# Kernel tuning notes

Hardware: AMD Instinct MI355X
Metric: run time of the kernel (lower is better)

Reference implementation:

```python
import jax, jax.numpy as jnp
import numpy as np

B, S, HID = 1, 2048, 2048
NH, NKV, D = 32, 8, 64
GROUPS = NH // NKV
THETA = 10000.0


def _rope_tables(seq_len, dim):
    inv_freq = 1.0 / (THETA ** (jnp.arange(0, dim, 2, dtype=jnp.float32) / dim))
    t = jnp.arange(seq_len, dtype=jnp.float32)
    freqs = jnp.outer(t, inv_freq)            # [S, D/2]
    emb = jnp.concatenate([freqs, freqs], axis=-1)  # [S, D]
    return jnp.cos(emb), jnp.sin(emb)


def _rotate_half(x):
    x1, x2 = jnp.split(x, 2, axis=-1)
    return jnp.concatenate([-x2, x1], axis=-1)


def setup_inputs() -> dict:
    key = jax.random.key(0)
    ks = jax.random.split(key, 8)
    hidden_states = jax.random.normal(ks[0], (B, S, HID), dtype=jnp.float32)
    # additive causal mask, 0 on/below diagonal, -1e9 above
    causal = jnp.tril(jnp.ones((S, S), dtype=bool))
    attention_mask = jnp.where(causal, 0.0, -1e9).astype(jnp.float32)[None, None]
    sc = 0.02
    Wq = sc * jax.random.normal(ks[1], (NH * D, HID), dtype=jnp.float32)
    bq = jnp.zeros((NH * D,), dtype=jnp.float32)
    Wk = sc * jax.random.normal(ks[2], (NKV * D, HID), dtype=jnp.float32)
    bk = jnp.zeros((NKV * D,), dtype=jnp.float32)
    Wv = sc * jax.random.normal(ks[3], (NKV * D, HID), dtype=jnp.float32)
    bv = jnp.zeros((NKV * D,), dtype=jnp.float32)
    Wo = sc * jax.random.normal(ks[4], (HID, NH * D), dtype=jnp.float32)
    return {"hidden_states": hidden_states, "attention_mask": attention_mask,
            "Wq": Wq, "bq": bq, "Wk": Wk, "bk": bk, "Wv": Wv, "bv": bv, "Wo": Wo}


def reference(hidden_states, attention_mask, Wq, bq, Wk, bk, Wv, bv, Wo):
    b, s, _ = hidden_states.shape
    q = (hidden_states @ Wq.T + bq).reshape(b, s, NH, D).transpose(0, 2, 1, 3)   # [B,NH,S,D]
    k = (hidden_states @ Wk.T + bk).reshape(b, s, NKV, D).transpose(0, 2, 1, 3)  # [B,NKV,S,D]
    v = (hidden_states @ Wv.T + bv).reshape(b, s, NKV, D).transpose(0, 2, 1, 3)
    cos, sin = _rope_tables(s, D)
    cos = cos[None, None]; sin = sin[None, None]
    q = q * cos + _rotate_half(q) * sin
    k = k * cos + _rotate_half(k) * sin
    # GQA: repeat KV heads to match query heads
    k = jnp.repeat(k, GROUPS, axis=1)  # [B,NH,S,D]
    v = jnp.repeat(v, GROUPS, axis=1)
    scores = jnp.einsum('bhqd,bhkd->bhqk', q, k) / jnp.sqrt(jnp.float32(D))
    scores = jnp.clip(scores, -50.0, 50.0)
    scores = scores + attention_mask
    probs = jax.nn.softmax(scores.astype(jnp.float32), axis=-1).astype(q.dtype)
    attn = jnp.einsum('bhqk,bhkd->bhqd', probs, v)
    attn = attn.transpose(0, 2, 1, 3).reshape(b, s, NH * D)
    return attn @ Wo.T
```

## Files before the change

kernel.cpp:

```cpp
#include <hip/hip_runtime.h>
#include <hip/hip_bf16.h>
#include <stdint.h>

typedef unsigned short u16;
typedef unsigned int u32;

#define S_LEN 2048
#define HID 2048
#define NH 32
#define NKV 8
#define HD 64
#define PIT 2080

using f32x4 = __attribute__((ext_vector_type(4))) float;
using bfrag = __attribute__((ext_vector_type(8))) short;

__device__ __forceinline__ float b2f(u16 u) {
  union { u32 i; float f; } c; c.i = ((u32)u) << 16; return c.f;
}
__device__ __forceinline__ u16 f2b(float f) {
  union { float f; u32 i; } c; c.f = f;
  u32 r = c.i + 0x7fffu + ((c.i >> 16) & 1u);
  return (u16)(r >> 16);
}
__device__ __forceinline__ uint4 cvt8(const float* __restrict__ p) {
  float4 a = *(const float4*)p;
  float4 b = *(const float4*)(p + 4);
  uint4 r;
  r.x = (u32)f2b(a.x) | ((u32)f2b(a.y) << 16);
  r.y = (u32)f2b(a.z) | ((u32)f2b(a.w) << 16);
  r.z = (u32)f2b(b.x) | ((u32)f2b(b.y) << 16);
  r.w = (u32)f2b(b.z) | ((u32)f2b(b.w) << 16);
  return r;
}

__device__ __forceinline__ void gl2lds16(const u16* g, u16* l) {
  __builtin_amdgcn_global_load_lds(
      (const __attribute__((address_space(1))) void*)g,
      (__attribute__((address_space(3))) void*)l,
      16, 0, 0);
}

#define WAITBAR(N) asm volatile("s_waitcnt vmcnt(" #N ")\ns_barrier" ::: "memory")

__global__ void conv_all(const float* __restrict__ hid, const float* __restrict__ Wq,
                         const float* __restrict__ Wk, const float* __restrict__ Wv,
                         u16* __restrict__ hidb, u16* __restrict__ Wqkvb) {
  int row = blockIdx.x;
  int col = threadIdx.x * 8;
  const float* src; u16* dst;
  if (row < 2048)      { src = hid + (size_t)row * 2048;          dst = hidb  + (size_t)row * PIT; }
  else if (row < 4096) { src = Wq + (size_t)(row - 2048) * 2048;  dst = Wqkvb + (size_t)(row - 2048) * PIT; }
  else if (row < 4608) { src = Wk + (size_t)(row - 4096) * 2048;  dst = Wqkvb + (size_t)(row - 4096 + 2048) * PIT; }
  else                 { src = Wv + (size_t)(row - 4608) * 2048;  dst = Wqkvb + (size_t)(row - 4608 + 2560) * PIT; }
  *(uint4*)(dst + col) = cvt8(src + col);
}

__global__ void conv_f2b_p(const float* __restrict__ in, u16* __restrict__ out, int n8) {
  int i = blockIdx.x * 256 + threadIdx.x;
  if (i >= n8) return;
  int row = i >> 8;
  int col = (i & 255) * 8;
  *(uint4*)(out + (size_t)row * PIT + col) = cvt8(in + (size_t)row * 2048 + col);
}

__global__ __launch_bounds__(256, 3) void gemm_qkv(
    const u16* __restrict__ A, const u16* __restrict__ B,
    const float* __restrict__ bq, const float* __restrict__ bk, const float* __restrict__ bv,
    u16* __restrict__ Qb, u16* __restrict__ Kb, u16* __restrict__ Vt)
{
  __shared__ __align__(16) u16 As[3 * 2048];
  __shared__ __align__(16) u16 Bs[3 * 4096];
  __shared__ __align__(16) u16 strip_s[4][16 * 72];

  const int tid  = threadIdx.x;
  const int m0   = blockIdx.y * 64;
  const int n0   = blockIdx.x * 128;
  const int lane = tid & 63;
  const int w    = tid >> 6;
  const int wm   = w >> 1, wn = w & 1;
  const int quad = lane >> 4, l16 = lane & 15;

  const int srow = tid >> 2;
  const int scol = (tid & 3) * 8;
  const u16* ga = A + (size_t)(m0 + srow) * PIT + scol;
  const u16* gb = B + (size_t)(n0 + srow) * PIT + scol;

#define STAGE_G(bi, k0)                                                         \
  do {                                                                          \
    gl2lds16(ga + (k0), As + (bi) * 2048 + tid * 8);                            \
    gl2lds16(gb + (k0), Bs + (bi) * 4096 + tid * 8);                            \
    gl2lds16(gb + (size_t)64 * PIT + (k0), Bs + (bi) * 4096 + 2048 + tid * 8);  \
  } while (0)

  f32x4 zero = {0.f, 0.f, 0.f, 0.f};
  f32x4 acc[2][4];
#pragma unroll
  for (int mi = 0; mi < 2; ++mi)
#pragma unroll
    for (int ni = 0; ni < 4; ++ni) acc[mi][ni] = zero;

  STAGE_G(0, 0);
  STAGE_G(1, 32);

  int cur = 0;
  for (int k = 0; k < 64; ++k) {
    if (k < 63) WAITBAR(3);
    else        WAITBAR(0);
    if (k + 2 < 64) {
      int nb = cur + 2; if (nb >= 3) nb -= 3;
      STAGE_G(nb, (k + 2) * 32);
    }
    const u16* as = As + cur * 2048;
    const u16* bs = Bs + cur * 4096;

    bfrag af[2], bf[4];
#pragma unroll
    for (int i = 0; i < 2; ++i)
      af[i] = *(const bfrag*)&as[(wm * 32 + i * 16 + l16) * 32 + quad * 8];
#pragma unroll
    for (int i = 0; i < 4; ++i)
      bf[i] = *(const bfrag*)&bs[(wn * 64 + i * 16 + l16) * 32 + quad * 8];
#pragma unroll
    for (int mi = 0; mi < 2; ++mi)
#pragma unroll
      for (int ni = 0; ni < 4; ++ni)
        acc[mi][ni] = __builtin_amdgcn_mfma_f32_16x16x32_bf16(af[mi], bf[ni], acc[mi][ni], 0, 0, 0);

    cur += 1; if (cur == 3) cur = 0;
  }
#undef STAGE_G

  u16* strip = strip_s[w];
  const int rr = lane >> 2;
  const int co = (lane & 3) * 8;

  if (n0 < 2048) {
#pragma unroll
    for (int mi = 0; mi < 2; ++mi) {
#pragma unroll
      for (int n01 = 0; n01 < 2; ++n01)
#pragma unroll
        for (int i = 0; i < 4; ++i) {
          int d  = n01 * 16 + l16;
          int c1 = n0 + wn * 64 + d;
          float x1 = acc[mi][n01][i]     + bq[c1];
          float x2 = acc[mi][n01 + 2][i] + bq[c1 + 32];
          float inv = exp2f(-(float)d * 0.41524101186092034f);
          float ang = (float)(m0 + wm * 32 + mi * 16 + quad * 4 + i) * inv;
          float cs = cosf(ang), sn = sinf(ang);
          strip[(quad * 4 + i) * 72 + d]      = f2b(x1 * cs - x2 * sn);
          strip[(quad * 4 + i) * 72 + d + 32] = f2b(x2 * cs + x1 * sn);
        }
      uint4 v0 = *(const uint4*)&strip[rr * 72 + co];
      uint4 v1 = *(const uint4*)&strip[rr * 72 + 32 + co];
      size_t gb2 = (size_t)(m0 + wm * 32 + mi * 16 + rr) * 2048 + n0 + wn * 64;
      *(uint4*)(Qb + gb2 + co)      = v0;
      *(uint4*)(Qb + gb2 + 32 + co) = v1;
    }
  } else if (n0 < 2560) {
    int cb = (n0 - 2048) + wn * 64;
#pragma unroll
    for (int mi = 0; mi < 2; ++mi) {
#pragma unroll
      for (int n01 = 0; n01 < 2; ++n01)
#pragma unroll
        for (int i = 0; i < 4; ++i) {
          int d  = n01 * 16 + l16;
          int cg = cb + d;
          float x1 = acc[mi][n01][i]     + bk[cg];
          float x2 = acc[mi][n01 + 2][i] + bk[cg + 32];
          float inv = exp2f(-(float)d * 0.41524101186092034f);
          float ang = (float)(m0 + wm * 32 + mi * 16 + quad * 4 + i) * inv;
          float cs = cosf(ang), sn = sinf(ang);
          strip[(quad * 4 + i) * 72 + d]      = f2b(x1 * cs - x2 * sn);
          strip[(quad * 4 + i) * 72 + d + 32] = f2b(x2 * cs + x1 * sn);
        }
      uint4 v0 = *(const uint4*)&strip[rr * 72 + co];
      uint4 v1 = *(const uint4*)&strip[rr * 72 + 32 + co];
      size_t gb2 = (size_t)(m0 + wm * 32 + mi * 16 + rr) * 512 + cb;
      *(uint4*)(Kb + gb2 + co)      = v0;
      *(uint4*)(Kb + gb2 + 32 + co) = v1;
    }
  } else {
    int cgb = (n0 - 2560) + wn * 64;
#pragma unroll
    for (int ni = 0; ni < 4; ++ni) {
      float bvv = bv[cgb + ni * 16 + l16];
#pragma unroll
      for (int mi = 0; mi < 2; ++mi)
#pragma unroll
        for (int i = 0; i < 4; ++i)
          strip[l16 * 72 + mi * 16 + quad * 4 + i] = f2b(acc[mi][ni][i] + bvv);
      uint4 v0 = *(const uint4*)&strip[rr * 72 + co];
      size_t gb2 = (size_t)(cgb + ni * 16 + rr) * PIT + m0 + wm * 32;
      *(uint4*)(Vt + gb2 + co) = v0;
    }
  }
}

__global__ __launch_bounds__(256, 3) void gemm_o(
    const u16* __restrict__ A, const u16* __restrict__ B, float* __restrict__ C)
{
  __shared__ __align__(16) u16 As[2 * 4096];
  __shared__ __align__(16) u16 Bs[2 * 8192];

  const int tid  = threadIdx.x;
  const int m0   = blockIdx.y * 64;
  const int n0   = blockIdx.x * 128;
  const int lane = tid & 63;
  const int w    = tid >> 6;
  const int wm   = w >> 1, wn = w & 1;
  const int quad = lane >> 4, l16 = lane & 15;

  const int sr = tid >> 3;
  const int sg = (tid & 7) ^ (sr & 7);
  const u16* gA = A + (size_t)(m0 + sr) * PIT + sg * 8;
  const u16* gB = B + (size_t)(n0 + sr) * PIT + sg * 8;

#define STAGE_O(bi, k0)                                                          \
  do {                                                                           \
    gl2lds16(gA + (k0),                    As + (bi) * 4096 + tid * 8);          \
    gl2lds16(gA + (size_t)32 * PIT + (k0), As + (bi) * 4096 + 2048 + tid * 8);   \
    gl2lds16(gB + (k0),                    Bs + (bi) * 8192 + tid * 8);          \
    gl2lds16(gB + (size_t)32 * PIT + (k0), Bs + (bi) * 8192 + 2048 + tid * 8);   \
    gl2lds16(gB + (size_t)64 * PIT + (k0), Bs + (bi) * 8192 + 4096 + tid * 8);   \
    gl2lds16(gB + (size_t)96 * PIT + (k0), Bs + (bi) * 8192 + 6144 + tid * 8);   \
  } while (0)

  f32x4 zero = {0.f, 0.f, 0.f, 0.f};
  f32x4 acc[2][4];
#pragma unroll
  for (int mi = 0; mi < 2; ++mi)
#pragma unroll
    for (int ni = 0; ni < 4; ++ni) acc[mi][ni] = zero;

  STAGE_O(0, 0);

  int cur = 0;
  for (int k = 0; k < 32; ++k) {
    WAITBAR(0);
    if (k + 1 < 32) STAGE_O(cur ^ 1, (k + 1) * 64);
    const u16* as = As + cur * 4096;
    const u16* bs = Bs + cur * 8192;

#pragma unroll
    for (int kk = 0; kk < 2; ++kk) {
      const int sA = ((kk * 4 + quad) ^ (l16 & 7)) * 8;
      bfrag af[2], bf[4];
#pragma unroll
      for (int i = 0; i < 2; ++i)
        af[i] = *(const bfrag*)&as[(wm * 32 + i * 16 + l16) * 64 + sA];
#pragma unroll
      for (int i = 0; i < 4; ++i)
        bf[i] = *(const bfrag*)&bs[(wn * 64 + i * 16 + l16) * 64 + sA];
#pragma unroll
      for (int mi = 0; mi < 2; ++mi)
#pragma unroll
        for (int ni = 0; ni < 4; ++ni)
          acc[mi][ni] = __builtin_amdgcn_mfma_f32_16x16x32_bf16(af[mi], bf[ni], acc[mi][ni], 0, 0, 0);
    }
    cur ^= 1;
  }
#undef STAGE_O

#pragma unroll
  for (int ni = 0; ni < 4; ++ni) {
    int col = n0 + wn * 64 + ni * 16 + l16;
#pragma unroll
    for (int mi = 0; mi < 2; ++mi)
#pragma unroll
      for (int i = 0; i < 4; ++i) {
        int row = m0 + wm * 32 + mi * 16 + quad * 4 + i;
        C[(size_t)row * 2048 + col] = acc[mi][ni][i];
      }
  }
}

#define SM_SC 0.18033688011112042f
#define SM_UB 72.134752044448169f

__global__ __launch_bounds__(256, 2) void attn_flash6(
    const u16* __restrict__ Qb, const u16* __restrict__ Kb,
    const u16* __restrict__ Vt, u16* __restrict__ Ab)
{
  __shared__ __align__(16) u16 Ks[3][64 * 64];
  __shared__ __align__(16) u16 Vs[3][64 * 64];
  __shared__ __align__(16) u16 Ps[4][16][72];

  const int h    = blockIdx.x;
  const int p    = blockIdx.y;
  const int kvh  = h >> 2;
  const int tid  = threadIdx.x;
  const int lane = tid & 63;
  const int w    = tid >> 6;
  const int quad = lane >> 4, l16 = lane & 15;

  const int qtA = 31 - p, qtB = p;
  const int nA  = qtA + 1;

  const int c0  = w * 128 + lane;
  const int r0  = c0 >> 3,        s0 = c0 & 7;
  const int r1  = (c0 + 64) >> 3, s1 = (c0 + 64) & 7;
  const int sg0 = s0 ^ (r0 & 7);
  const int sg1 = s1 ^ (r1 & 7);
  const u16* Ksrc0 = Kb + (size_t)r0 * 512 + kvh * 64 + sg0 * 8;
  const u16* Ksrc1 = Kb + (size_t)r1 * 512 + kvh * 64 + sg1 * 8;
  const u16* Vsrc0 = Vt + (size_t)(kvh * 64 + r0) * PIT + sg0 * 8;
  const u16* Vsrc1 = Vt + (size_t)(kvh * 64 + r1) * PIT + sg1 * 8;

#define STAGEKV(buf, kb)                                                        \
  do {                                                                          \
    gl2lds16(Ksrc0 + (size_t)(kb) * 32768, &Ks[buf][0] + c0 * 8);               \
    gl2lds16(Ksrc1 + (size_t)(kb) * 32768, &Ks[buf][0] + (c0 + 64) * 8);        \
    gl2lds16(Vsrc0 + (kb) * 64,            &Vs[buf][0] + c0 * 8);               \
    gl2lds16(Vsrc1 + (kb) * 64,            &Vs[buf][0] + (c0 + 64) * 8);        \
  } while (0)

  STAGEKV(0, 0);
  STAGEKV(1, 1);

  bfrag qfA0, qfA1, qfB0, qfB1;
  {
    const u16* qa = Qb + (size_t)(qtA * 64 + w * 16 + l16) * 2048 + h * 64 + quad * 8;
    const u16* qb = Qb + (size_t)(qtB * 64 + w * 16 + l16) * 2048 + h * 64 + quad * 8;
    qfA0 = *(const bfrag*)qa;  qfA1 = *(const bfrag*)(qa + 32);
    qfB0 = *(const bfrag*)qb;  qfB1 = *(const bfrag*)(qb + 32);
  }
  bfrag q0 = qfA0, q1 = qfA1;

  f32x4 zero = {0.f, 0.f, 0.f, 0.f};
  f32x4 o_acc[4];
  float lpart[4];
#pragma unroll
  for (int nb = 0; nb < 4; ++nb) { o_acc[nb] = zero; lpart[nb] = 0.f; }

  const int swz = (l16 & 7) * 8;
  int qt = qtA;
  int cur = 0;

  for (int t = 0; t < 33; ++t) {
    if (t < 32) WAITBAR(4);
    else        WAITBAR(0);
    if (t + 2 < 33) {
      int kb2 = (t + 2 < nA) ? (t + 2) : (t + 2 - nA);
      int b3 = cur + 2; if (b3 >= 3) b3 -= 3;
      STAGEKV(b3, kb2);
    }
    if (t == nA) { q0 = qfB0; q1 = qfB1; qt = qtB; }

    const u16* ks = &Ks[cur][0];
    const u16* vs = &Vs[cur][0];

    bfrag kf0[4], kf1[4];
#pragma unroll
    for (int nb = 0; nb < 4; ++nb) {
      int row = (nb * 16 + l16) * 64;
      kf0[nb] = *(const bfrag*)&ks[row + ((quad * 8) ^ swz)];
      kf1[nb] = *(const bfrag*)&ks[row + ((32 + quad * 8) ^ swz)];
    }

    const bool diag = (t == nA - 1) || (t == 32);

    f32x4 s_acc[4];
#pragma unroll
    for (int nb = 0; nb < 4; ++nb) {
      s_acc[nb] = __builtin_amdgcn_mfma_f32_16x16x32_bf16(q0, kf0[nb], zero, 0, 0, 0);
      s_acc[nb] = __builtin_amdgcn_mfma_f32_16x16x32_bf16(q1, kf1[nb], s_acc[nb], 0, 0, 0);
    }
    if (diag) {
#pragma unroll
      for (int nb = 0; nb < 4; ++nb)
#pragma unroll
        for (int i = 0; i < 4; ++i) {
          float u = s_acc[nb][i] * SM_SC;
          u = fminf(SM_UB, fmaxf(-SM_UB, u));
          bool msk = (nb * 16 + l16 > w * 16 + quad * 4 + i);
          float pr = msk ? 0.0f : __builtin_amdgcn_exp2f(u);
          lpart[i] += pr;
          Ps[w][quad * 4 + i][nb * 16 + l16] = f2b(pr);
        }
    } else {
#pragma unroll
      for (int nb = 0; nb < 4; ++nb)
#pragma unroll
        for (int i = 0; i < 4; ++i) {
          float u = s_acc[nb][i] * SM_SC;
          u = fminf(SM_UB, fmaxf(-SM_UB, u));
          float pr = __builtin_amdgcn_exp2f(u);
          lpart[i] += pr;
          Ps[w][quad * 4 + i][nb * 16 + l16] = f2b(pr);
        }
    }

    bfrag vf0[4], vf1[4];
#pragma unroll
    for (int nb = 0; nb < 4; ++nb) {
      int row = (nb * 16 + l16) * 64;
      vf0[nb] = *(const bfrag*)&vs[row + ((quad * 8) ^ swz)];
      vf1[nb] = *(const bfrag*)&vs[row + ((32 + quad * 8) ^ swz)];
    }
    {
      bfrag pf0 = *(const bfrag*)&Ps[w][l16][quad * 8];
      bfrag pf1 = *(const bfrag*)&Ps[w][l16][32 + quad * 8];
#pragma unroll
      for (int nb = 0; nb < 4; ++nb) {
        o_acc[nb] = __builtin_amdgcn_mfma_f32_16x16x32_bf16(pf0, vf0[nb], o_acc[nb], 0, 0, 0);
        o_acc[nb] = __builtin_amdgcn_mfma_f32_16x16x32_bf16(pf1, vf1[nb], o_acc[nb], 0, 0, 0);
      }
    }

    if (diag) {
#pragma unroll
      for (int off = 1; off < 16; off <<= 1)
#pragma unroll
        for (int i = 0; i < 4; ++i)
          lpart[i] += __shfl_xor(lpart[i], off, 64);
#pragma unroll
      for (int i = 0; i < 4; ++i) {
        float inv = 1.0f / lpart[i];
        size_t rbase = (size_t)(qt * 64 + w * 16 + quad * 4 + i) * PIT + h * 64;
#pragma unroll
        for (int nb = 0; nb < 4; ++nb)
          Ab[rbase + nb * 16 + l16] = f2b(o_acc[nb][i] * inv);
      }
#pragma unroll
      for (int nb = 0; nb < 4; ++nb) { o_acc[nb] = zero; lpart[nb] = 0.f; }
    }

    cur += 1; if (cur == 3) cur = 0;
  }
}

extern "C" void kernel_launch(void* const* d_in, const int* in_sizes, int n_in,
                              void* d_out, int out_size, void* d_ws, size_t ws_size,
                              hipStream_t stream) {
  const float* hid = (const float*)d_in[0];
  const float* Wq = (const float*)d_in[2];
  const float* bq = (const float*)d_in[3];
  const float* Wk = (const float*)d_in[4];
  const float* bk = (const float*)d_in[5];
  const float* Wv = (const float*)d_in[6];
  const float* bv = (const float*)d_in[7];
  const float* Wo = (const float*)d_in[8];

  u16* hidb  = (u16*)d_ws;
  u16* Wqkvb = hidb + (size_t)2048 * PIT;
  u16* Qb    = Wqkvb + (size_t)3072 * PIT;
  u16* Kb    = Qb + 4194304;
  u16* Vt    = Kb + 1048576;
  u16* Wob   = hidb;
  u16* Ab    = Wqkvb;
  float* Ob  = (float*)d_out;

  conv_all<<<5120, 256, 0, stream>>>(hid, Wq, Wk, Wv, hidb, Wqkvb);

  gemm_qkv<<<dim3(24, 32), 256, 0, stream>>>(hidb, Wqkvb, bq, bk, bv, Qb, Kb, Vt);

  conv_f2b_p<<<2048, 256, 0, stream>>>(Wo, Wob, 524288);

  attn_flash6<<<dim3(32, 16), 256, 0, stream>>>(Qb, Kb, Vt, Ab);

  gemm_o<<<dim3(16, 32), 256, 0, stream>>>(Ab, Wob, Ob);
}
```

Before: 240.1 us.

## Double-buffer QKV GEMM with BK=64 XOR-swizzled LDS tiles

Replaces the three-stage BK=32 pipeline in the QKV projection GEMM with a two-stage BK=64 pipeline, halving the number of barriers per K. LDS rows are XOR-swizzled at 16-byte granularity to avoid bank conflicts on the wider 64-element rows. The epilogue strip buffer now reuses the A tile region after a sync, which keeps LDS usage bounded. The cost is less prefetch depth, since it waits for all outstanding loads each iteration, and the LDS footprint may limit occupancy.

```diff
diff --git a/kernel.cpp b/kernel.cpp
--- a/kernel.cpp
+++ b/kernel.cpp
@@ -69,9 +69,8 @@
     const float* __restrict__ bq, const float* __restrict__ bk, const float* __restrict__ bv,
     u16* __restrict__ Qb, u16* __restrict__ Kb, u16* __restrict__ Vt)
 {
-  __shared__ __align__(16) u16 As[3 * 2048];
-  __shared__ __align__(16) u16 Bs[3 * 4096];
-  __shared__ __align__(16) u16 strip_s[4][16 * 72];
+  __shared__ __align__(16) u16 As[2 * 4096];
+  __shared__ __align__(16) u16 Bs[2 * 8192];
 
   const int tid  = threadIdx.x;
   const int m0   = blockIdx.y * 64;
@@ -81,16 +80,19 @@
   const int wm   = w >> 1, wn = w & 1;
   const int quad = lane >> 4, l16 = lane & 15;
 
-  const int srow = tid >> 2;
-  const int scol = (tid & 3) * 8;
-  const u16* ga = A + (size_t)(m0 + srow) * PIT + scol;
-  const u16* gb = B + (size_t)(n0 + srow) * PIT + scol;
-
-#define STAGE_G(bi, k0)                                                         \
-  do {                                                                          \
-    gl2lds16(ga + (k0), As + (bi) * 2048 + tid * 8);                            \
-    gl2lds16(gb + (k0), Bs + (bi) * 4096 + tid * 8);                            \
-    gl2lds16(gb + (size_t)64 * PIT + (k0), Bs + (bi) * 4096 + 2048 + tid * 8);  \
+  const int sr = tid >> 3;
+  const int sg = (tid & 7) ^ (sr & 7);
+  const u16* gA = A + (size_t)(m0 + sr) * PIT + sg * 8;
+  const u16* gB = B + (size_t)(n0 + sr) * PIT + sg * 8;
+
+#define STAGE_G(bi, k0)                                                          \
+  do {                                                                           \
+    gl2lds16(gA + (k0),                    As + (bi) * 4096 + tid * 8);          \
+    gl2lds16(gA + (size_t)32 * PIT + (k0), As + (bi) * 4096 + 2048 + tid * 8);   \
+    gl2lds16(gB + (k0),                    Bs + (bi) * 8192 + tid * 8);          \
+    gl2lds16(gB + (size_t)32 * PIT + (k0), Bs + (bi) * 8192 + 2048 + tid * 8);   \
+    gl2lds16(gB + (size_t)64 * PIT + (k0), Bs + (bi) * 8192 + 4096 + tid * 8);   \
+    gl2lds16(gB + (size_t)96 * PIT + (k0), Bs + (bi) * 8192 + 6144 + tid * 8);   \
   } while (0)
 
   f32x4 zero = {0.f, 0.f, 0.f, 0.f};
@@ -101,37 +103,36 @@
     for (int ni = 0; ni < 4; ++ni) acc[mi][ni] = zero;
 
   STAGE_G(0, 0);
-  STAGE_G(1, 32);
 
   int cur = 0;
-  for (int k = 0; k < 64; ++k) {
-    if (k < 63) WAITBAR(3);
-    else        WAITBAR(0);
-    if (k + 2 < 64) {
-      int nb = cur + 2; if (nb >= 3) nb -= 3;
-      STAGE_G(nb, (k + 2) * 32);
-    }
-    const u16* as = As + cur * 2048;
-    const u16* bs = Bs + cur * 4096;
-
-    bfrag af[2], bf[4];
-#pragma unroll
-    for (int i = 0; i < 2; ++i)
-      af[i] = *(const bfrag*)&as[(wm * 32 + i * 16 + l16) * 32 + quad * 8];
-#pragma unroll
-    for (int i = 0; i < 4; ++i)
-      bf[i] = *(const bfrag*)&bs[(wn * 64 + i * 16 + l16) * 32 + quad * 8];
-#pragma unroll
-    for (int mi = 0; mi < 2; ++mi)
-#pragma unroll
-      for (int ni = 0; ni < 4; ++ni)
-        acc[mi][ni] = __builtin_amdgcn_mfma_f32_16x16x32_bf16(af[mi], bf[ni], acc[mi][ni], 0, 0, 0);
-
-    cur += 1; if (cur == 3) cur = 0;
+  for (int k = 0; k < 32; ++k) {
+    WAITBAR(0);
+    if (k + 1 < 32) STAGE_G(cur ^ 1, (k + 1) * 64);
+    const u16* as = As + cur * 4096;
+    const u16* bs = Bs + cur * 8192;
+
+#pragma unroll
+    for (int kk = 0; kk < 2; ++kk) {
+      const int sA = ((kk * 4 + quad) ^ (l16 & 7)) * 8;
+      bfrag af[2], bf[4];
+#pragma unroll
+      for (int i = 0; i < 2; ++i)
+        af[i] = *(const bfrag*)&as[(wm * 32 + i * 16 + l16) * 64 + sA];
+#pragma unroll
+      for (int i = 0; i < 4; ++i)
+        bf[i] = *(const bfrag*)&bs[(wn * 64 + i * 16 + l16) * 64 + sA];
+#pragma unroll
+      for (int mi = 0; mi < 2; ++mi)
+#pragma unroll
+        for (int ni = 0; ni < 4; ++ni)
+          acc[mi][ni] = __builtin_amdgcn_mfma_f32_16x16x32_bf16(af[mi], bf[ni], acc[mi][ni], 0, 0, 0);
+    }
+    cur ^= 1;
   }
 #undef STAGE_G
 
-  u16* strip = strip_s[w];
+  __syncthreads();
+  u16* strip = As + w * 1152;
   const int rr = lane >> 2;
   const int co = (lane & 3) * 8;
 
```

Measured after the change: 233.2 us. 1.03x faster.
